# Kernel tuning notes

Hardware: AMD Instinct MI355X
Metric: run time of the kernel (lower is better)

The kernel has to match this reference:

```python
import math
import jax, jax.numpy as jnp
import numpy as np

NUM_BUCKETS = 32
MAX_DISTANCE = 128
N_HEADS = 16
D_KV = 64


def _relative_position_bucket(relative_position, num_buckets=NUM_BUCKETS, max_distance=MAX_DISTANCE):
    # bidirectional (encoder) version, faithful to T5Attention._relative_position_bucket
    nb = num_buckets // 2
    rel_buckets = (relative_position > 0).astype(jnp.int32) * nb
    rp = jnp.abs(relative_position)
    max_exact = nb // 2
    is_small = rp < max_exact
    # log-spaced buckets for large distances; clamp arg of log to >=1 to avoid -inf
    rp_large = max_exact + (
        jnp.log(jnp.maximum(rp, 1).astype(jnp.float32) / max_exact)
        / math.log(max_distance / max_exact)
        * (nb - max_exact)
    ).astype(jnp.int32)
    rp_large = jnp.minimum(rp_large, nb - 1)
    return rel_buckets + jnp.where(is_small, rp, rp_large)


def setup_inputs() -> dict:
    key = jax.random.key(0)
    ks = jax.random.split(key, 6)
    B, S, D = 2, 2048, 1024
    scale = 0.02
    return {
        "hidden_states": jax.random.normal(ks[0], (B, S, D), dtype=jnp.float32),
        "Wq": jax.random.normal(ks[1], (D, N_HEADS * D_KV), dtype=jnp.float32) * scale,
        "Wk": jax.random.normal(ks[2], (D, N_HEADS * D_KV), dtype=jnp.float32) * scale,
        "Wv": jax.random.normal(ks[3], (D, N_HEADS * D_KV), dtype=jnp.float32) * scale,
        "Wo": jax.random.normal(ks[4], (N_HEADS * D_KV, D), dtype=jnp.float32) * scale,
        "rel_bias": jax.random.normal(ks[5], (NUM_BUCKETS, N_HEADS), dtype=jnp.float32),
    }


def reference(hidden_states, Wq, Wk, Wv, Wo, rel_bias):
    B, S, D = hidden_states.shape
    H, dk = N_HEADS, D_KV
    q = (hidden_states @ Wq).reshape(B, S, H, dk)
    k = (hidden_states @ Wk).reshape(B, S, H, dk)
    v = (hidden_states @ Wv).reshape(B, S, H, dk)

    pos = jnp.arange(S)
    relative_position = pos[None, :] - pos[:, None]          # [S_q, S_k]
    buckets = _relative_position_bucket(relative_position)    # [S_q, S_k]
    bias = rel_bias[buckets].transpose(2, 0, 1)               # [H, S_q, S_k]

    # T5 attention: NO 1/sqrt(d) scaling
    scores = jnp.einsum('bqhd,bkhd->bhqk', q, k) + bias[None]
    attn = jax.nn.softmax(scores, axis=-1)
    ctx = jnp.einsum('bhqk,bkhd->bqhd', attn, v).reshape(B, S, H * dk)
    return ctx @ Wo
```

## Files before the change

kernel.cpp:

```cpp
#include <hip/hip_runtime.h>
#include <stdint.h>

#define S_LEN 2048
#define NH 16
#define NB_DELTA (2*S_LEN-1)
#define PST 72

typedef __attribute__((ext_vector_type(8))) __bf16 bf16x8;
typedef __attribute__((ext_vector_type(4))) float f32x4;

__device__ __forceinline__ unsigned short f2bf(float f){
    union { float f; unsigned int u; } v; v.f = f;
    unsigned int u = v.u;
    return (unsigned short)((u + 0x7FFFu + ((u >> 16) & 1u)) >> 16);
}
__device__ __forceinline__ unsigned short f2bf_fast(float f){
    union { float f; unsigned int u; } v; v.f = f;
    return (unsigned short)((v.u + 0x8000u) >> 16);
}
__device__ __forceinline__ float bf2f(unsigned short u){
    union { unsigned int u; float f; } v; v.u = ((unsigned int)u) << 16;
    return v.f;
}

__device__ __forceinline__ void gload16(const void* g, void* l){
    __builtin_amdgcn_global_load_lds(
        (const __attribute__((address_space(1))) void*)(uintptr_t)g,
        (__attribute__((address_space(3))) void*)(uintptr_t)l, 16, 0, 0);
}

__global__ __launch_bounds__(256) void prep_kernel(
    const float* __restrict__ hs, unsigned short* __restrict__ hsb,
    const float* __restrict__ W0, const float* __restrict__ W1,
    const float* __restrict__ W2, const float* __restrict__ W3,
    unsigned short* __restrict__ D0, unsigned short* __restrict__ D1,
    unsigned short* __restrict__ D2, unsigned short* __restrict__ D3,
    const float* __restrict__ rel_bias, float* __restrict__ biasT){
    if (blockIdx.z == 4) {
        int bi = blockIdx.y * 32 + blockIdx.x;
        for (int it = 0; it < 4; it++) {
            int i = bi * 4096 + it * 1024 + threadIdx.x * 4;
            float4 f = *(const float4*)(hs + i);
            ushort4 o;
            o.x = f2bf(f.x); o.y = f2bf(f.y); o.z = f2bf(f.z); o.w = f2bf(f.w);
            *(ushort4*)(hsb + i) = o;
        }
        if (bi < 16) {
            int t = bi * 256 + threadIdx.x;
            if (t < NB_DELTA) {
                int delta = t - (S_LEN - 1);
                int bucket = (delta > 0) ? 16 : 0;
                int a = delta < 0 ? -delta : delta;
                int b;
                if (a < 8) b = a;
                else {
                    int bl = 33 - __builtin_clz(a * a);
                    b = bl < 15 ? bl : 15;
                }
                bucket += b;
                for (int h = 0; h < NH; h++)
                    biasT[h * NB_DELTA + t] = rel_bias[bucket * NH + h];
            }
        }
        return;
    }
    const float* src; unsigned short* dst;
    switch (blockIdx.z) {
        case 0: src = W0; dst = D0; break;
        case 1: src = W1; dst = D1; break;
        case 2: src = W2; dst = D2; break;
        default: src = W3; dst = D3; break;
    }
    __shared__ float tile[32][33];
    int bx = blockIdx.x, by = blockIdx.y;
    int tx = threadIdx.x & 31, ty = threadIdx.x >> 5;
    for (int i = 0; i < 4; i++)
        tile[ty + 8*i][tx] = src[(size_t)(by*32 + ty + 8*i) * 1024 + bx*32 + tx];
    __syncthreads();
    for (int i = 0; i < 4; i++)
        dst[(size_t)(bx*32 + ty + 8*i) * 1024 + by*32 + tx] = f2bf(tile[tx][ty + 8*i]);
}

template<int MODE, int BM>
__global__ __launch_bounds__(256) void gemm_bt_kernel(const unsigned short* __restrict__ A,
                                                      const unsigned short* __restrict__ BT,
                                                      float* __restrict__ C0,
                                                      unsigned short* __restrict__ C1,
                                                      int Kdim, int ldc){
    constexpr int IT = BM / 32;
    __shared__ __align__(16) unsigned short As[BM * 64];
    __shared__ __align__(16) unsigned short Bs[128 * 64];
    const int t = threadIdx.x;
    const int wave = t >> 6, lane = t & 63;
    const int quad = lane >> 4, l16 = lane & 15;
    const int wm = (wave >> 1) * (BM / 2), wn = (wave & 1) * 64;
    const size_t row0 = (size_t)blockIdx.y * BM, col0 = (size_t)blockIdx.x * 128;

    const int srow8 = lane >> 3;
    const int gg = (lane & 7) ^ srow8;
    const unsigned short* gA = A  + (row0 + wave * 8 + srow8) * (size_t)Kdim + gg * 8;
    const unsigned short* gB = BT + (col0 + wave * 8 + srow8) * (size_t)Kdim + gg * 8;

    f32x4 acc[IT][4] = {};

    for (int kt = 0; kt < Kdim; kt += 64) {
        for (int p = 0; p < BM / 32; p++)
            gload16(gA + (size_t)(p * 32) * Kdim + kt, &As[(p * 32 + wave * 8) * 64]);
        for (int p = 0; p < 4; p++)
            gload16(gB + (size_t)(p * 32) * Kdim + kt, &Bs[(p * 32 + wave * 8) * 64]);
        __syncthreads();
        bf16x8 a[2][IT], b[2][4];
        for (int ks = 0; ks < 2; ks++) {
            for (int i = 0; i < IT; i++)
                a[ks][i] = *(const bf16x8*)(&As[(wm + i*16 + l16) * 64 + (((ks*4 + quad) ^ (l16 & 7)) * 8)]);
            for (int j = 0; j < 4; j++)
                b[ks][j] = *(const bf16x8*)(&Bs[(wn + j*16 + l16) * 64 + (((ks*4 + quad) ^ (l16 & 7)) * 8)]);
        }
        for (int ks = 0; ks < 2; ks++)
            for (int i = 0; i < IT; i++)
                for (int j = 0; j < 4; j++)
                    acc[i][j] = __builtin_amdgcn_mfma_f32_16x16x32_bf16(a[ks][i], b[ks][j], acc[i][j], 0, 0, 0);
        __syncthreads();
    }
    for (int i = 0; i < IT; i++)
        for (int j = 0; j < 4; j++) {
            size_t r0 = row0 + wm + i*16 + quad*4;
            size_t c  = col0 + wn + j*16 + l16;
            if (MODE == 0) {
                for (int r = 0; r < 4; r++)
                    C0[(r0 + r) * ldc + c] = acc[i][j][r];
            } else {
                for (int r = 0; r < 4; r++)
                    C1[(r0 + r) * ldc + c] = f2bf(acc[i][j][r]);
            }
        }
}

__global__ __launch_bounds__(256) void vtrans_kernel(const unsigned short* __restrict__ qkv,
                                                     unsigned short* __restrict__ vt){
    __shared__ unsigned short tile[64][72];
    const int v0 = blockIdx.x * 64, s0 = blockIdx.y * 64, b = blockIdx.z;
    const int tx = threadIdx.x & 7, ty = threadIdx.x >> 3;
    for (int i = 0; i < 2; i++)
        *(int4*)&tile[ty + 32*i][tx * 8] =
            *(const int4*)(qkv + (size_t)(b * 2048 + s0 + ty + 32*i) * 3072 + 2048 + v0 + tx * 8);
    __syncthreads();
    for (int i = 0; i < 2; i++) {
        int v = ty + 32*i;
        int sl = tx * 8;
        ushort4 o0, o1;
        o0.x = tile[sl+0][v]; o0.y = tile[sl+1][v]; o0.z = tile[sl+2][v]; o0.w = tile[sl+3][v];
        o1.x = tile[sl+4][v]; o1.y = tile[sl+5][v]; o1.z = tile[sl+6][v]; o1.w = tile[sl+7][v];
        unsigned short* dst = vt + (size_t)(b * 1024 + v0 + v) * 2048 + s0 + sl;
        *(ushort4*)dst = o0; *(ushort4*)(dst + 4) = o1;
    }
}

__global__ __launch_bounds__(256, 4) void flash7_kernel(
    const unsigned short* __restrict__ qkv,
    const unsigned short* __restrict__ vt,
    const float* __restrict__ biasT,
    unsigned short* __restrict__ ctxpb,
    float* __restrict__ rsbuf)
{
    const int qt = blockIdx.x, h = blockIdx.y;
    const int b = blockIdx.z >> 1, ck = blockIdx.z & 1;
    const int kt0 = ck << 10;
    const int t = threadIdx.x;
    const int w = t >> 6, lane = t & 63, quad = lane >> 4, l16 = lane & 15;
    const int q0 = qt * 128;

    __shared__ __align__(16) unsigned short Ks[64 * 64];
    __shared__ __align__(16) unsigned short Vs[64 * 64];
    __shared__ __align__(16) unsigned short Pb[128 * PST];
    __shared__ float bias_s[192];

    for (int s = 0; s < 4; s++) {
        int g = t + s * 256;
        int r = g >> 3, c = (g & 7) * 8;
        *(int4*)&Pb[r * PST + c] =
            *(const int4*)(qkv + (size_t)(b * S_LEN + q0 + r) * 3072 + h * 64 + c);
    }
    __syncthreads();
    bf16x8 qb[2][2];
    for (int nt = 0; nt < 2; nt++)
        for (int ks = 0; ks < 2; ks++)
            qb[ks][nt] = *(const bf16x8*)&Pb[(w * 32 + nt * 16 + l16) * PST + ks * 32 + quad * 8];

    float rsum[2] = {0.f, 0.f};
    f32x4 ctx[4][2] = {};

    const float* biasRow = biasT + h * NB_DELTA + 2047;

    const int srow8 = lane >> 3;
    const int gg = (lane & 7) ^ srow8;
    const int swz = ((l16 & 7) * 8);

    for (int kt = kt0; kt < kt0 + 1024; kt += 64) {
        __syncthreads();
        {
            const unsigned short* kb = qkv + (size_t)(b * S_LEN + kt + w * 8 + srow8) * 3072 + 1024 + h * 64 + gg * 8;
            const unsigned short* vb = vt + (size_t)(b * 1024 + h * 64 + w * 8 + srow8) * 2048 + kt + gg * 8;
            gload16(kb,                         &Ks[(w * 8) * 64]);
            gload16(kb + (size_t)32 * 3072,     &Ks[(32 + w * 8) * 64]);
            gload16(vb,                         &Vs[(w * 8) * 64]);
            gload16(vb + (size_t)32 * 2048,     &Vs[(32 + w * 8) * 64]);
            if (t < 192) bias_s[t] = biasRow[kt - q0 - 127 + t] - 16.0f;
        }
        __syncthreads();

        f32x4 st[4][2] = {};
        for (int ks = 0; ks < 2; ks++)
            for (int nb = 0; nb < 4; nb++) {
                bf16x8 ka = *(const bf16x8*)&Ks[(nb * 16 + l16) * 64 + (((ks * 4 + quad) * 8) ^ swz)];
                st[nb][0] = __builtin_amdgcn_mfma_f32_16x16x32_bf16(ka, qb[ks][0], st[nb][0], 0, 0, 0);
                st[nb][1] = __builtin_amdgcn_mfma_f32_16x16x32_bf16(ka, qb[ks][1], st[nb][1], 0, 0, 0);
            }
        for (int nt = 0; nt < 2; nt++) {
            const int ib = quad * 4 + 127 - w * 32 - nt * 16 - l16;
            float rs = 0.f;
            for (int nb = 0; nb < 4; nb++) {
                float e0 = __expf(st[nb][nt][0] + bias_s[ib + nb * 16 + 0]);
                float e1 = __expf(st[nb][nt][1] + bias_s[ib + nb * 16 + 1]);
                float e2 = __expf(st[nb][nt][2] + bias_s[ib + nb * 16 + 2]);
                float e3 = __expf(st[nb][nt][3] + bias_s[ib + nb * 16 + 3]);
                rs += (e0 + e1) + (e2 + e3);
                ushort4 pk;
                pk.x = f2bf_fast(e0); pk.y = f2bf_fast(e1);
                pk.z = f2bf_fast(e2); pk.w = f2bf_fast(e3);
                *(ushort4*)&Pb[(w * 32 + nt * 16 + l16) * PST + nb * 16 + quad * 4] = pk;
            }
            rsum[nt] += rs;
        }
        for (int ks = 0; ks < 2; ks++) {
            bf16x8 pb0 = *(const bf16x8*)&Pb[(w * 32 + l16) * PST + ks * 32 + quad * 8];
            bf16x8 pb1 = *(const bf16x8*)&Pb[(w * 32 + 16 + l16) * PST + ks * 32 + quad * 8];
            for (int nd = 0; nd < 4; nd++) {
                bf16x8 va = *(const bf16x8*)&Vs[(nd * 16 + l16) * 64 + (((ks * 4 + quad) * 8) ^ swz)];
                ctx[nd][0] = __builtin_amdgcn_mfma_f32_16x16x32_bf16(va, pb0, ctx[nd][0], 0, 0, 0);
                ctx[nd][1] = __builtin_amdgcn_mfma_f32_16x16x32_bf16(va, pb1, ctx[nd][1], 0, 0, 0);
            }
        }
    }
    unsigned short* cp = ctxpb + (size_t)ck * 4096 * 1024;
    for (int nt = 0; nt < 2; nt++) {
        float rs = rsum[nt];
        rs += __shfl_xor(rs, 16, 64);
        rs += __shfl_xor(rs, 32, 64);
        int row = b * S_LEN + q0 + w * 32 + nt * 16 + l16;
        if (quad == 0) rsbuf[((size_t)ck * 4096 + row) * 16 + h] = rs;
        for (int nd = 0; nd < 4; nd++) {
            ushort4 pk;
            pk.x = f2bf(ctx[nd][nt][0]); pk.y = f2bf(ctx[nd][nt][1]);
            pk.z = f2bf(ctx[nd][nt][2]); pk.w = f2bf(ctx[nd][nt][3]);
            *(ushort4*)&cp[(size_t)row * 1024 + h * 64 + nd * 16 + quad * 4] = pk;
        }
    }
}

__global__ __launch_bounds__(256) void combine_kernel(const unsigned short* __restrict__ ctxpb,
                                                      const float* __restrict__ rsbuf,
                                                      unsigned short* __restrict__ ctxb){
    int e = blockIdx.x * 256 + threadIdx.x;
    int row = e >> 8;
    int c4 = (e & 255) * 4;
    int h = c4 >> 6;
    float l = rsbuf[(size_t)row * 16 + h] + rsbuf[((size_t)4096 + row) * 16 + h];
    ushort4 a  = *(const ushort4*)&ctxpb[(size_t)row * 1024 + c4];
    ushort4 b2 = *(const ushort4*)&ctxpb[(size_t)4096 * 1024 + (size_t)row * 1024 + c4];
    float inv = 1.f / l;
    ushort4 o;
    o.x = f2bf((bf2f(a.x) + bf2f(b2.x)) * inv);
    o.y = f2bf((bf2f(a.y) + bf2f(b2.y)) * inv);
    o.z = f2bf((bf2f(a.z) + bf2f(b2.z)) * inv);
    o.w = f2bf((bf2f(a.w) + bf2f(b2.w)) * inv);
    *(ushort4*)&ctxb[(size_t)row * 1024 + c4] = o;
}

extern "C" void kernel_launch(void* const* d_in, const int* in_sizes, int n_in,
                              void* d_out, int out_size, void* d_ws, size_t ws_size,
                              hipStream_t stream) {
    const float* hs       = (const float*)d_in[0];
    const float* Wq       = (const float*)d_in[1];
    const float* Wk       = (const float*)d_in[2];
    const float* Wv       = (const float*)d_in[3];
    const float* Wo       = (const float*)d_in[4];
    const float* rel_bias = (const float*)d_in[5];
    float* out = (float*)d_out;

    char* ws = (char*)d_ws;
    float* biasT          = (float*)ws;           ws += 262144;
    unsigned short* hsb   = (unsigned short*)ws;  ws += 8388608;
    unsigned short* WT    = (unsigned short*)ws;  ws += 6291456;
    unsigned short* WoT   = (unsigned short*)ws;  ws += 2097152;
    unsigned short* qkvb  = (unsigned short*)ws;  ws += 25165824;
    unsigned short* Vtg   = (unsigned short*)ws;  ws += 8388608;
    unsigned short* ctxb  = (unsigned short*)ws;  ws += 8388608;
    unsigned short* ctxpb = (unsigned short*)ws;  ws += 16777216;
    float* rsbuf          = (float*)ws;

    prep_kernel<<<dim3(32, 32, 5), 256, 0, stream>>>(
        hs, hsb, Wq, Wk, Wv, Wo,
        WT, WT + 1024 * 1024, WT + 2 * 1024 * 1024, WoT, rel_bias, biasT);

    gemm_bt_kernel<1, 128><<<dim3(24, 32), 256, 0, stream>>>(hsb, WT, nullptr, qkvb, 1024, 3072);
    vtrans_kernel<<<dim3(16, 32, 2), 256, 0, stream>>>(qkvb, Vtg);
    flash7_kernel<<<dim3(S_LEN / 128, NH, 4), 256, 0, stream>>>(qkvb, Vtg, biasT, ctxpb, rsbuf);
    combine_kernel<<<4096, 256, 0, stream>>>(ctxpb, rsbuf, ctxb);
    gemm_bt_kernel<0, 64><<<dim3(8, 64), 256, 0, stream>>>(ctxb, WoT, out, nullptr, 1024, 1024);
}
```

Before: 207.6 us.

## Fold log2e into Q, use exp2, skip bias loads in constant-bucket tiles

The QKV GEMM epilogue now pre-scales Q by log2(e), so the attention kernel can call the hardware exp2 instead of __expf. Key tiles far from the diagonal, where every T5 bucket saturates to bucket 15 or 31, use a per-head scalar bias and skip the shared-memory bias load and lookups. bf16 packing now goes through paired round-to-nearest conversions, and the QKV GEMM tile height drops from 128 to 64 with twice as many blocks. Rounding P with RN instead of the fast round adds a little ALU work, and the smaller GEMM tiles trade data reuse for more parallelism.

```diff
diff --git a/kernel.cpp b/kernel.cpp
--- a/kernel.cpp
+++ b/kernel.cpp
@@ -1,10 +1,12 @@
 #include <hip/hip_runtime.h>
+#include <hip/hip_bf16.h>
 #include <stdint.h>
 
 #define S_LEN 2048
 #define NH 16
 #define NB_DELTA (2*S_LEN-1)
 #define PST 72
+#define LOG2E 1.4426950408889634f
 
 typedef __attribute__((ext_vector_type(8))) __bf16 bf16x8;
 typedef __attribute__((ext_vector_type(4))) float f32x4;
@@ -14,14 +16,21 @@
     unsigned int u = v.u;
     return (unsigned short)((u + 0x7FFFu + ((u >> 16) & 1u)) >> 16);
 }
-__device__ __forceinline__ unsigned short f2bf_fast(float f){
-    union { float f; unsigned int u; } v; v.f = f;
-    return (unsigned short)((v.u + 0x8000u) >> 16);
-}
 __device__ __forceinline__ float bf2f(unsigned short u){
     union { unsigned int u; float f; } v; v.u = ((unsigned int)u) << 16;
     return v.f;
 }
+__device__ __forceinline__ unsigned int pkbf(float a, float b){
+    __hip_bfloat162 h = __float22bfloat162_rn(float2{a, b});
+    unsigned int u;
+    __builtin_memcpy(&u, &h, 4);
+    return u;
+}
+#if __has_builtin(__builtin_amdgcn_exp2f)
+__device__ __forceinline__ float fexp2(float x){ return __builtin_amdgcn_exp2f(x); }
+#else
+__device__ __forceinline__ float fexp2(float x){ return __expf(x * 0.69314718056f); }
+#endif
 
 __device__ __forceinline__ void gload16(const void* g, void* l){
     __builtin_amdgcn_global_load_lds(
@@ -130,8 +139,9 @@
                 for (int r = 0; r < 4; r++)
                     C0[(r0 + r) * ldc + c] = acc[i][j][r];
             } else {
+                float qs = (c < 1024) ? LOG2E : 1.0f;
                 for (int r = 0; r < 4; r++)
-                    C1[(r0 + r) * ldc + c] = f2bf(acc[i][j][r]);
+                    C1[(r0 + r) * ldc + c] = f2bf(acc[i][j][r] * qs);
             }
         }
 }
@@ -156,10 +166,11 @@
     }
 }
 
-__global__ __launch_bounds__(256, 4) void flash7_kernel(
+__global__ __launch_bounds__(256, 4) void flash10_kernel(
     const unsigned short* __restrict__ qkv,
     const unsigned short* __restrict__ vt,
     const float* __restrict__ biasT,
+    const float* __restrict__ rel_bias,
     unsigned short* __restrict__ ctxpb,
     float* __restrict__ rsbuf)
 {
@@ -175,6 +186,9 @@
     __shared__ __align__(16) unsigned short Pb[128 * PST];
     __shared__ float bias_s[192];
 
+    const float b15 = (rel_bias[15 * NH + h] - 16.f) * LOG2E;
+    const float b31 = (rel_bias[31 * NH + h] - 16.f) * LOG2E;
+
     for (int s = 0; s < 4; s++) {
         int g = t + s * 256;
         int r = g >> 3, c = (g & 7) * 8;
@@ -197,15 +211,17 @@
     const int swz = ((l16 & 7) * 8);
 
     for (int kt = kt0; kt < kt0 + 1024; kt += 64) {
+        const int off = kt - q0;
+        const bool cst = (off >= 255) || (off <= -191);
         __syncthreads();
         {
             const unsigned short* kb = qkv + (size_t)(b * S_LEN + kt + w * 8 + srow8) * 3072 + 1024 + h * 64 + gg * 8;
             const unsigned short* vb = vt + (size_t)(b * 1024 + h * 64 + w * 8 + srow8) * 2048 + kt + gg * 8;
-            gload16(kb,                         &Ks[(w * 8) * 64]);
-            gload16(kb + (size_t)32 * 3072,     &Ks[(32 + w * 8) * 64]);
-            gload16(vb,                         &Vs[(w * 8) * 64]);
-            gload16(vb + (size_t)32 * 2048,     &Vs[(32 + w * 8) * 64]);
-            if (t < 192) bias_s[t] = biasRow[kt - q0 - 127 + t] - 16.0f;
+            gload16(kb,                     &Ks[(w * 8) * 64]);
+            gload16(kb + (size_t)32 * 3072, &Ks[(32 + w * 8) * 64]);
+            gload16(vb,                     &Vs[(w * 8) * 64]);
+            gload16(vb + (size_t)32 * 2048, &Vs[(32 + w * 8) * 64]);
+            if (!cst && t < 192) bias_s[t] = (biasRow[off - 127 + t] - 16.f) * LOG2E;
         }
         __syncthreads();
 
@@ -216,19 +232,26 @@
                 st[nb][0] = __builtin_amdgcn_mfma_f32_16x16x32_bf16(ka, qb[ks][0], st[nb][0], 0, 0, 0);
                 st[nb][1] = __builtin_amdgcn_mfma_f32_16x16x32_bf16(ka, qb[ks][1], st[nb][1], 0, 0, 0);
             }
+        const float bc = (off > 0) ? b31 : b15;
         for (int nt = 0; nt < 2; nt++) {
             const int ib = quad * 4 + 127 - w * 32 - nt * 16 - l16;
             float rs = 0.f;
             for (int nb = 0; nb < 4; nb++) {
-                float e0 = __expf(st[nb][nt][0] + bias_s[ib + nb * 16 + 0]);
-                float e1 = __expf(st[nb][nt][1] + bias_s[ib + nb * 16 + 1]);
-                float e2 = __expf(st[nb][nt][2] + bias_s[ib + nb * 16 + 2]);
-                float e3 = __expf(st[nb][nt][3] + bias_s[ib + nb * 16 + 3]);
+                float e0, e1, e2, e3;
+                if (cst) {
+                    e0 = fexp2(st[nb][nt][0] + bc);
+                    e1 = fexp2(st[nb][nt][1] + bc);
+                    e2 = fexp2(st[nb][nt][2] + bc);
+                    e3 = fexp2(st[nb][nt][3] + bc);
+                } else {
+                    e0 = fexp2(st[nb][nt][0] + bias_s[ib + nb * 16 + 0]);
+                    e1 = fexp2(st[nb][nt][1] + bias_s[ib + nb * 16 + 1]);
+                    e2 = fexp2(st[nb][nt][2] + bias_s[ib + nb * 16 + 2]);
+                    e3 = fexp2(st[nb][nt][3] + bias_s[ib + nb * 16 + 3]);
+                }
                 rs += (e0 + e1) + (e2 + e3);
-                ushort4 pk;
-                pk.x = f2bf_fast(e0); pk.y = f2bf_fast(e1);
-                pk.z = f2bf_fast(e2); pk.w = f2bf_fast(e3);
-                *(ushort4*)&Pb[(w * 32 + nt * 16 + l16) * PST + nb * 16 + quad * 4] = pk;
+                uint2 pk; pk.x = pkbf(e0, e1); pk.y = pkbf(e2, e3);
+                *(uint2*)&Pb[(w * 32 + nt * 16 + l16) * PST + nb * 16 + quad * 4] = pk;
             }
             rsum[nt] += rs;
         }
@@ -250,10 +273,10 @@
         int row = b * S_LEN + q0 + w * 32 + nt * 16 + l16;
         if (quad == 0) rsbuf[((size_t)ck * 4096 + row) * 16 + h] = rs;
         for (int nd = 0; nd < 4; nd++) {
-            ushort4 pk;
-            pk.x = f2bf(ctx[nd][nt][0]); pk.y = f2bf(ctx[nd][nt][1]);
-            pk.z = f2bf(ctx[nd][nt][2]); pk.w = f2bf(ctx[nd][nt][3]);
-            *(ushort4*)&cp[(size_t)row * 1024 + h * 64 + nd * 16 + quad * 4] = pk;
+            uint2 pk;
+            pk.x = pkbf(ctx[nd][nt][0], ctx[nd][nt][1]);
+            pk.y = pkbf(ctx[nd][nt][2], ctx[nd][nt][3]);
+            *(uint2*)&cp[(size_t)row * 1024 + h * 64 + nd * 16 + quad * 4] = pk;
         }
     }
 }
@@ -269,12 +292,10 @@
     ushort4 a  = *(const ushort4*)&ctxpb[(size_t)row * 1024 + c4];
     ushort4 b2 = *(const ushort4*)&ctxpb[(size_t)4096 * 1024 + (size_t)row * 1024 + c4];
     float inv = 1.f / l;
-    ushort4 o;
-    o.x = f2bf((bf2f(a.x) + bf2f(b2.x)) * inv);
-    o.y = f2bf((bf2f(a.y) + bf2f(b2.y)) * inv);
-    o.z = f2bf((bf2f(a.z) + bf2f(b2.z)) * inv);
-    o.w = f2bf((bf2f(a.w) + bf2f(b2.w)) * inv);
-    *(ushort4*)&ctxb[(size_t)row * 1024 + c4] = o;
+    uint2 o;
+    o.x = pkbf((bf2f(a.x) + bf2f(b2.x)) * inv, (bf2f(a.y) + bf2f(b2.y)) * inv);
+    o.y = pkbf((bf2f(a.z) + bf2f(b2.z)) * inv, (bf2f(a.w) + bf2f(b2.w)) * inv);
+    *(uint2*)&ctxb[(size_t)row * 1024 + c4] = o;
 }
 
 extern "C" void kernel_launch(void* const* d_in, const int* in_sizes, int n_in,
@@ -303,9 +324,9 @@
         hs, hsb, Wq, Wk, Wv, Wo,
         WT, WT + 1024 * 1024, WT + 2 * 1024 * 1024, WoT, rel_bias, biasT);
 
-    gemm_bt_kernel<1, 128><<<dim3(24, 32), 256, 0, stream>>>(hsb, WT, nullptr, qkvb, 1024, 3072);
+    gemm_bt_kernel<1, 64><<<dim3(24, 64), 256, 0, stream>>>(hsb, WT, nullptr, qkvb, 1024, 3072);
     vtrans_kernel<<<dim3(16, 32, 2), 256, 0, stream>>>(qkvb, Vtg);
-    flash7_kernel<<<dim3(S_LEN / 128, NH, 4), 256, 0, stream>>>(qkvb, Vtg, biasT, ctxpb, rsbuf);
+    flash10_kernel<<<dim3(S_LEN / 128, NH, 4), 256, 0, stream>>>(qkvb, Vtg, biasT, rel_bias, ctxpb, rsbuf);
     combine_kernel<<<4096, 256, 0, stream>>>(ctxpb, rsbuf, ctxb);
     gemm_bt_kernel<0, 64><<<dim3(8, 64), 256, 0, stream>>>(ctxb, WoT, out, nullptr, 1024, 1024);
 }
```

Result: faster. 203.0 us (-2.2%).
